# Kernel tuning notes

Hardware: AMD Instinct MI355X
Metric: run time of the kernel (lower is better)

The kernel has to match this reference:

```python
import jax, jax.numpy as jnp
import numpy as np

D_MODEL = 1024
H = 16
D_K = D_MODEL // H
B, S = 4, 2048


def setup_inputs() -> dict:
    key = jax.random.key(0)
    ks = jax.random.split(key, 12)
    s = 1.0 / np.sqrt(D_MODEL)
    inp = {
        "q": jax.random.normal(ks[0], (B, S, D_MODEL), jnp.float32),
        "k": jax.random.normal(ks[1], (B, S, D_MODEL), jnp.float32),
        "v": jax.random.normal(ks[2], (B, S, D_MODEL), jnp.float32),
        "mask": jax.random.randint(ks[3], (1, 1, S, S), 0, 2, jnp.int32),
        # torch nn.Linear convention: weight [out, in], y = x @ W.T + b
        "w_q": jax.random.uniform(ks[4], (D_MODEL, D_MODEL), jnp.float32, -s, s),
        "b_q": jax.random.uniform(ks[5], (D_MODEL,), jnp.float32, -s, s),
        "w_k": jax.random.uniform(ks[6], (D_MODEL, D_MODEL), jnp.float32, -s, s),
        "b_k": jax.random.uniform(ks[7], (D_MODEL,), jnp.float32, -s, s),
        "w_v": jax.random.uniform(ks[8], (D_MODEL, D_MODEL), jnp.float32, -s, s),
        "b_v": jax.random.uniform(ks[9], (D_MODEL,), jnp.float32, -s, s),
        "w_o": jax.random.uniform(ks[10], (D_MODEL, D_MODEL), jnp.float32, -s, s),
        "b_o": jax.random.uniform(ks[11], (D_MODEL,), jnp.float32, -s, s),
    }
    return inp


def _split_heads(x):
    b, s, _ = x.shape
    return x.reshape(b, s, H, D_K).transpose(0, 2, 1, 3)  # [B,H,S,Dk]


def reference(q, k, v, mask, w_q, b_q, w_k, b_k, w_v, b_v, w_o, b_o):
    query = _split_heads(q @ w_q.T + b_q)
    key = _split_heads(k @ w_k.T + b_k)
    value = _split_heads(v @ w_v.T + b_v)
    scores = jnp.einsum("bhqd,bhkd->bhqk", query, key) / jnp.sqrt(
        jnp.asarray(D_K, query.dtype))
    scores = jnp.where(mask == 0, jnp.asarray(-1e9, scores.dtype), scores)
    attn = jax.nn.softmax(scores, axis=-1)  # dropout p=0 (eval) -> identity
    x = jnp.einsum("bhqk,bhkd->bhqd", attn, value)
    x = x.transpose(0, 2, 1, 3).reshape(q.shape[0], -1, H * D_K)
    return x @ w_o.T + b_o
```

## Files before the change

kernel.cpp:

```cpp
#include <hip/hip_runtime.h>

typedef __bf16 bf16_t;
typedef __bf16 bf16x4 __attribute__((ext_vector_type(4)));
typedef __bf16 bf16x8 __attribute__((ext_vector_type(8)));
typedef float f32x4 __attribute__((ext_vector_type(4)));
typedef float f32x16 __attribute__((ext_vector_type(16)));
typedef unsigned int uint;
typedef uint uint4v __attribute__((ext_vector_type(4)));

#define CSCALE 0.18033688011112042f

static __device__ __forceinline__ bf16_t f2bf(float f) {
  unsigned u = __builtin_bit_cast(unsigned, f);
  u = (u + 0x7fff + ((u >> 16) & 1)) >> 16;
  unsigned short h = (unsigned short)u;
  return __builtin_bit_cast(bf16_t, h);
}
static __device__ __forceinline__ uint cvt_pk(float a, float b) {
  uint r;
  asm("v_cvt_pk_bf16_f32 %0, %1, %2" : "=v"(r) : "v"(a), "v"(b));
  return r;
}

#define GLD_LDS(g, l) \
  __builtin_amdgcn_global_load_lds((const __attribute__((address_space(1))) void*)(g), \
                                   (__attribute__((address_space(3))) void*)(l), 16, 0, 0)
#define VMCNT(n) asm volatile("s_waitcnt vmcnt(" #n ")" ::: "memory")
#define RAW_BARRIER() do { __builtin_amdgcn_s_barrier(); __builtin_amdgcn_sched_barrier(0); } while (0)

__global__ void cvt4_f2b(const float* __restrict__ a, const float* __restrict__ b,
                         const float* __restrict__ c, const float* __restrict__ d,
                         bf16_t* __restrict__ oa, bf16_t* __restrict__ ob,
                         bf16_t* __restrict__ oc, bf16_t* __restrict__ od) {
  int i = blockIdx.x * 256 + threadIdx.x;
  const float* src = a;
  bf16_t* dst = oa;
  int w = i >> 18;
  i &= 262143;
  if (w == 1) { src = b; dst = ob; }
  else if (w == 2) { src = c; dst = oc; }
  else if (w == 3) { src = d; dst = od; }
  const float4 f = reinterpret_cast<const float4*>(src)[i];
  bf16x4 o;
  o[0] = f2bf(f.x); o[1] = f2bf(f.y); o[2] = f2bf(f.z); o[3] = f2bf(f.w);
  reinterpret_cast<bf16x4*>(dst)[i] = o;
}

__global__ void mask_bits_k(const int* __restrict__ m, uint* __restrict__ out) {
  int i = blockIdx.x * 256 + threadIdx.x;
  int q = i & 2047, t = i >> 11;
  const int* mrow = m + (size_t)q * 2048 + t * 32;
  uint bits = 0;
#pragma unroll
  for (int j = 0; j < 16; ++j) {
    int r0 = (j & 3) + 8 * (j >> 2);
    bits |= (mrow[r0] ? 1u : 0u) << j;
    bits |= (mrow[r0 + 4] ? 1u : 0u) << (16 + j);
  }
  out[(size_t)t * 2048 + q] = bits;
}

__global__ __launch_bounds__(256, 2) void qkv_gemm(
    const float* __restrict__ qA, const float* __restrict__ kA, const float* __restrict__ vA,
    const bf16_t* __restrict__ wq, const bf16_t* __restrict__ wk, const bf16_t* __restrict__ wv,
    const float* __restrict__ bq, const float* __restrict__ bk, const float* __restrict__ bv,
    bf16_t* __restrict__ Qp, bf16_t* __restrict__ Kp, bf16_t* __restrict__ Vt) {
  constexpr int K = 1024, N = 1024;
  __shared__ __align__(16) float Asf[3][128 * 32];
  __shared__ __align__(16) bf16_t Bs[3][128 * 32];
  const int z = blockIdx.z;
  const float* A = (z == 0) ? qA : (z == 1) ? kA : vA;
  const bf16_t* W = (z == 0) ? wq : (z == 1) ? wk : wv;
  const float* bias = (z == 0) ? bq : (z == 1) ? bk : bv;

  const int tid = threadIdx.x;
  const int lane = tid & 63;
  const int wv_ = tid >> 6;
  const int wm = (wv_ >> 1) * 64, wn = (wv_ & 1) * 64;
  const int l15 = lane & 15, lhi = lane >> 4;
  const int bm = blockIdx.x, bn = blockIdx.y;

  const int rA = tid >> 3;
  const float* gA = A + (size_t)(bm * 128 + rA) * K + ((tid & 7) ^ (rA & 7)) * 4;
  const int rB = tid >> 2;
  const bf16_t* gB = W + (size_t)(bn * 128 + rB) * K + ((tid & 3) ^ (rB & 3)) * 8;

  f32x4 acc[4][4] = {};

  auto STAGE = [&](int t, int buf) {
#pragma unroll
    for (int c2 = 0; c2 < 4; ++c2)
      GLD_LDS(gA + (size_t)c2 * 32 * K + t * 32, (char*)&Asf[buf][0] + c2 * 4096 + wv_ * 1024);
#pragma unroll
    for (int c2 = 0; c2 < 2; ++c2)
      GLD_LDS(gB + (size_t)c2 * 64 * K + t * 32, (char*)&Bs[buf][0] + c2 * 4096 + wv_ * 1024);
  };
  auto COMPUTE = [&](int buf) {
    bf16x8 af[4], bfv[4];
#pragma unroll
    for (int i = 0; i < 4; ++i) {
      int arow = wm + i * 16 + l15;
      f32x4 a0 = *reinterpret_cast<const f32x4*>(
          (const char*)&Asf[buf][0] + arow * 128 + (((2 * lhi) ^ (arow & 7)) * 16));
      f32x4 a1 = *reinterpret_cast<const f32x4*>(
          (const char*)&Asf[buf][0] + arow * 128 + (((2 * lhi + 1) ^ (arow & 7)) * 16));
      uint4v ua;
      ua[0] = cvt_pk(a0[0], a0[1]);
      ua[1] = cvt_pk(a0[2], a0[3]);
      ua[2] = cvt_pk(a1[0], a1[1]);
      ua[3] = cvt_pk(a1[2], a1[3]);
      af[i] = __builtin_bit_cast(bf16x8, ua);
    }
#pragma unroll
    for (int j = 0; j < 4; ++j) {
      int brow = wn + j * 16 + l15;
      bfv[j] = *reinterpret_cast<const bf16x8*>(
          (const char*)&Bs[buf][0] + brow * 64 + ((lhi ^ (brow & 3)) * 16));
    }
#pragma unroll
    for (int i = 0; i < 4; ++i)
#pragma unroll
      for (int j = 0; j < 4; ++j)
        acc[i][j] = __builtin_amdgcn_mfma_f32_16x16x32_bf16(af[i], bfv[j], acc[i][j], 0, 0, 0);
  };

  STAGE(0, 0);
  STAGE(1, 1);
#pragma unroll 1
  for (int tt = 0; tt < 30; tt += 3) {
    VMCNT(6); RAW_BARRIER(); COMPUTE(0); STAGE(tt + 2, 2);
    VMCNT(6); RAW_BARRIER(); COMPUTE(1); STAGE(tt + 3, 0);
    VMCNT(6); RAW_BARRIER(); COMPUTE(2); STAGE(tt + 4, 1);
  }
  VMCNT(6); RAW_BARRIER(); COMPUTE(0);
  VMCNT(0); RAW_BARRIER(); COMPUTE(1);

#pragma unroll
  for (int i = 0; i < 4; ++i) {
#pragma unroll
    for (int j = 0; j < 4; ++j) {
      int n = bn * 128 + wn + j * 16 + l15;
      float bv2 = bias[n];
#pragma unroll
      for (int r = 0; r < 4; ++r) {
        int m = bm * 128 + wm + i * 16 + lhi * 4 + r;
        float val = acc[i][j][r] + bv2;
        if (z == 0) {
          Qp[(size_t)m * N + n] = f2bf(val * CSCALE);
        } else if (z == 1) {
          Kp[(size_t)m * N + n] = f2bf(val);
        } else {
          int b = m >> 11, s = m & 2047;
          Vt[((size_t)b * 1024 + n) * 2048 + s] = f2bf(val);
        }
      }
    }
  }
}

__global__ __launch_bounds__(256, 2) void gemm_o(
    const bf16_t* __restrict__ A, const bf16_t* __restrict__ Bw,
    const float* __restrict__ bias, float* __restrict__ Cout) {
  constexpr int K = 1024, N = 1024;
  __shared__ __align__(16) bf16_t As[3][128 * 32];
  __shared__ __align__(16) bf16_t Bs[3][128 * 32];
  const int tid = threadIdx.x;
  const int lane = tid & 63;
  const int wv_ = tid >> 6;
  const int wm = (wv_ >> 1) * 64, wn = (wv_ & 1) * 64;
  const int l15 = lane & 15, lhi = lane >> 4;
  const int bm = blockIdx.x, bn = blockIdx.y;
  const int rB = tid >> 2;
  const bf16_t* ga = A + (size_t)(bm * 128 + rB) * K + ((tid & 3) ^ (rB & 3)) * 8;
  const bf16_t* gb = Bw + (size_t)(bn * 128 + rB) * K + ((tid & 3) ^ (rB & 3)) * 8;
  f32x4 acc[4][4] = {};

  auto STAGE = [&](int t, int buf) {
#pragma unroll
    for (int c2 = 0; c2 < 2; ++c2) {
      GLD_LDS(ga + (size_t)c2 * 64 * K + t * 32, (char*)&As[buf][0] + c2 * 4096 + wv_ * 1024);
      GLD_LDS(gb + (size_t)c2 * 64 * K + t * 32, (char*)&Bs[buf][0] + c2 * 4096 + wv_ * 1024);
    }
  };
  auto COMPUTE = [&](int buf) {
    bf16x8 af[4], bfv[4];
#pragma unroll
    for (int i = 0; i < 4; ++i) {
      int arow = wm + i * 16 + l15;
      af[i] = *reinterpret_cast<const bf16x8*>(
          (const char*)&As[buf][0] + arow * 64 + ((lhi ^ (arow & 3)) * 16));
    }
#pragma unroll
    for (int j = 0; j < 4; ++j) {
      int brow = wn + j * 16 + l15;
      bfv[j] = *reinterpret_cast<const bf16x8*>(
          (const char*)&Bs[buf][0] + brow * 64 + ((lhi ^ (brow & 3)) * 16));
    }
#pragma unroll
    for (int i = 0; i < 4; ++i)
#pragma unroll
      for (int j = 0; j < 4; ++j)
        acc[i][j] = __builtin_amdgcn_mfma_f32_16x16x32_bf16(af[i], bfv[j], acc[i][j], 0, 0, 0);
  };

  STAGE(0, 0);
  STAGE(1, 1);
#pragma unroll 1
  for (int tt = 0; tt < 30; tt += 3) {
    VMCNT(4); RAW_BARRIER(); COMPUTE(0); STAGE(tt + 2, 2);
    VMCNT(4); RAW_BARRIER(); COMPUTE(1); STAGE(tt + 3, 0);
    VMCNT(4); RAW_BARRIER(); COMPUTE(2); STAGE(tt + 4, 1);
  }
  VMCNT(4); RAW_BARRIER(); COMPUTE(0);
  VMCNT(0); RAW_BARRIER(); COMPUTE(1);

#pragma unroll
  for (int i = 0; i < 4; ++i)
#pragma unroll
    for (int j = 0; j < 4; ++j) {
      int n = bn * 128 + wn + j * 16 + l15;
      float bv2 = bias[n];
#pragma unroll
      for (int r = 0; r < 4; ++r) {
        int m = bm * 128 + wm + i * 16 + lhi * 4 + r;
        Cout[(size_t)m * N + n] = acc[i][j][r] + bv2;
      }
    }
}

static __device__ __forceinline__ f32x16 qk_tile(const bf16_t* Kbuf, const bf16x8 qf[4],
                                                 int l31, int h) {
  f32x16 s = {};
  __builtin_amdgcn_s_setprio(1);
#pragma unroll
  for (int c = 0; c < 4; ++c) {
    bf16x8 kf = *reinterpret_cast<const bf16x8*>(Kbuf + l31 * 64 + ((h + 2 * c) ^ (l31 & 7)) * 8);
    s = __builtin_amdgcn_mfma_f32_32x32x16_bf16(kf, qf[c], s, 0, 0, 0);
  }
  __builtin_amdgcn_s_setprio(0);
  return s;
}

static __device__ __forceinline__ void softmax_tile(
    const f32x16& sv, uint mb, int h, f32x16& o0, f32x16& o1,
    float& mrun, float& lsum, bf16x8& pa0, bf16x8& pa1) {
  const uint mbh = mb >> (h << 4);
  float a0 = fmaxf(fmaxf(sv[0], sv[1]), sv[2]);
  float a1 = fmaxf(fmaxf(sv[3], sv[4]), sv[5]);
  float a2 = fmaxf(fmaxf(sv[6], sv[7]), sv[8]);
  float a3 = fmaxf(fmaxf(sv[9], sv[10]), sv[11]);
  float a4 = fmaxf(fmaxf(sv[12], sv[13]), sv[14]);
  float b0 = fmaxf(fmaxf(a0, a1), a2);
  float mt = fmaxf(fmaxf(b0, fmaxf(a3, a4)), sv[15]);
  if (!__all(mt - mrun <= 8.0f)) {
    float mtf = fmaxf(mt, __shfl_xor(mt, 32));
    float mnew = fmaxf(mrun, mtf);
    float alpha = __builtin_amdgcn_exp2f(mrun - mnew);
    lsum *= alpha;
#pragma unroll
    for (int r = 0; r < 16; ++r) {
      float ar = __shfl(alpha, (r & 3) + 8 * (r >> 2) + 4 * h);
      o0[r] *= ar; o1[r] *= ar;
    }
    mrun = mnew;
  }
  float p[16];
#pragma unroll
  for (int r = 0; r < 16; ++r) {
    float pv = __builtin_amdgcn_exp2f(sv[r] - mrun);
    uint smask = (uint)__builtin_amdgcn_sbfe((int)mbh, r, 1);
    p[r] = __builtin_bit_cast(float, __builtin_bit_cast(uint, pv) & smask);
  }
  float t0 = p[0] + p[1], t1 = p[2] + p[3], t2 = p[4] + p[5], t3 = p[6] + p[7];
  float t4 = p[8] + p[9], t5 = p[10] + p[11], t6 = p[12] + p[13], t7 = p[14] + p[15];
  t0 += t1; t2 += t3; t4 += t5; t6 += t7;
  lsum += (t0 + t2) + (t4 + t6);
  uint dw[8];
#pragma unroll
  for (int i = 0; i < 8; ++i) dw[i] = cvt_pk(p[2 * i], p[2 * i + 1]);
  uint e0 = (uint)__shfl_xor((int)(h ? dw[0] : dw[2]), 32);
  uint e1 = (uint)__shfl_xor((int)(h ? dw[1] : dw[3]), 32);
  uint e2 = (uint)__shfl_xor((int)(h ? dw[4] : dw[6]), 32);
  uint e3 = (uint)__shfl_xor((int)(h ? dw[5] : dw[7]), 32);
  uint4v ua0 = {h ? e0 : dw[0], h ? e1 : dw[1], h ? dw[2] : e0, h ? dw[3] : e1};
  uint4v ua1 = {h ? e2 : dw[4], h ? e3 : dw[5], h ? dw[6] : e2, h ? dw[7] : e3};
  pa0 = __builtin_bit_cast(bf16x8, ua0);
  pa1 = __builtin_bit_cast(bf16x8, ua1);
}

static __device__ __forceinline__ void pv_tile(const bf16_t* Vbuf, bf16x8 pa0, bf16x8 pa1,
                                               int l31, int h, f32x16& o0, f32x16& o1) {
  const int sw = l31 & 3;
  bf16x8 v00 = *reinterpret_cast<const bf16x8*>(Vbuf + l31 * 32 + ((h ^ sw) * 8));
  bf16x8 v01 = *reinterpret_cast<const bf16x8*>(Vbuf + l31 * 32 + (((2 + h) ^ sw) * 8));
  bf16x8 v10 = *reinterpret_cast<const bf16x8*>(Vbuf + (32 + l31) * 32 + ((h ^ sw) * 8));
  bf16x8 v11 = *reinterpret_cast<const bf16x8*>(Vbuf + (32 + l31) * 32 + (((2 + h) ^ sw) * 8));
  __builtin_amdgcn_s_setprio(1);
  o0 = __builtin_amdgcn_mfma_f32_32x32x16_bf16(pa0, v00, o0, 0, 0, 0);
  o0 = __builtin_amdgcn_mfma_f32_32x32x16_bf16(pa1, v01, o0, 0, 0, 0);
  o1 = __builtin_amdgcn_mfma_f32_32x32x16_bf16(pa0, v10, o1, 0, 0, 0);
  o1 = __builtin_amdgcn_mfma_f32_32x32x16_bf16(pa1, v11, o1, 0, 0, 0);
  __builtin_amdgcn_s_setprio(0);
}

__global__ __launch_bounds__(256, 4) void attn_kernel(
    const bf16_t* __restrict__ Qp, const bf16_t* __restrict__ Kp,
    const bf16_t* __restrict__ Vt, const uint* __restrict__ maskbits,
    bf16_t* __restrict__ Xb) {
  constexpr int S = 2048, D = 1024;
  __shared__ __align__(16) bf16_t Ks[2][32][64];
  __shared__ __align__(16) bf16_t Vs[2][64][32];
  const int tid = threadIdx.x;
  const int wv_ = tid >> 6, lane = tid & 63;
  const int l31 = lane & 31, h = lane >> 5;
  const int blk = blockIdx.x;
  const int bh = blk & 63, qt4 = blk >> 6;
  const int b = bh >> 4, hd = bh & 15;
  const int q0 = qt4 * 128 + wv_ * 32;

  const int rK = tid >> 3;
  const bf16_t* gK = Kp + ((size_t)b * S + rK) * D + hd * 64 + ((tid & 7) ^ (rK & 7)) * 8;
  const int rV = tid >> 2;
  const bf16_t* gV = Vt + ((size_t)b * 1024 + hd * 64 + rV) * (size_t)S + ((tid & 3) ^ (rV & 3)) * 8;
  char* ldsK0 = (char*)&Ks[0][0][0] + wv_ * 1024;
  char* ldsK1 = (char*)&Ks[1][0][0] + wv_ * 1024;
  char* ldsV0 = (char*)&Vs[0][0][0] + wv_ * 1024;
  char* ldsV1 = (char*)&Vs[1][0][0] + wv_ * 1024;

  const bf16_t* qbase = Qp + (size_t)(b * S + q0 + l31) * D + hd * 64 + h * 8;
  bf16x8 qf[4];
#pragma unroll
  for (int c = 0; c < 4; ++c)
    qf[c] = *reinterpret_cast<const bf16x8*>(qbase + 16 * c);

  const uint* mbase = maskbits + q0 + l31;

  f32x16 o0 = {}, o1 = {};
  float mrun = 0.f, lsum = 0.f;
  bf16x8 pa0, pa1;

  GLD_LDS(gK, ldsK0);
  GLD_LDS(gK + (size_t)32 * D, ldsK1);
  GLD_LDS(gV, ldsV0);
  uint mb0 = mbase[0];
  __syncthreads();
  {
    f32x16 s = qk_tile(&Ks[0][0][0], qf, l31, h);
    softmax_tile(s, mb0, h, o0, o1, mrun, lsum, pa0, pa1);
  }

  auto body = [&](int j, char* ldsK_st, char* ldsV_st, const bf16_t* Kq,
                  const bf16_t* Vp, bool stageK) {
    if (stageK) GLD_LDS(gK + (size_t)(j + 2) * 32 * D, ldsK_st);
    GLD_LDS(gV + (size_t)(j + 1) * 32, ldsV_st);
    uint mbn = mbase[(size_t)(j + 1) * 2048];
    f32x16 s = qk_tile(Kq, qf, l31, h);
    pv_tile(Vp, pa0, pa1, l31, h, o0, o1);
    softmax_tile(s, mbn, h, o0, o1, mrun, lsum, pa0, pa1);
    __syncthreads();
  };

#pragma unroll 1
  for (int jj = 0; jj < 31; ++jj) {
    const int j = 2 * jj;
    body(j,     ldsK0, ldsV1, &Ks[1][0][0], &Vs[0][0][0], true);
    body(j + 1, ldsK1, ldsV0, &Ks[0][0][0], &Vs[1][0][0], true);
  }
  body(62, ldsK0, ldsV1, &Ks[1][0][0], &Vs[0][0][0], false);
  pv_tile(&Vs[1][0][0], pa0, pa1, l31, h, o0, o1);

  lsum += __shfl_xor(lsum, 32);
  float linv = __builtin_amdgcn_rcpf(lsum);
  bf16_t* xrow = Xb + (size_t)(b * S + q0) * D + hd * 64 + l31;
#pragma unroll
  for (int r = 0; r < 16; ++r) {
    int qrow = (r & 3) + 8 * (r >> 2) + 4 * h;
    float lr = __shfl(linv, qrow);
    xrow[(size_t)qrow * D] = f2bf(o0[r] * lr);
    xrow[(size_t)qrow * D + 32] = f2bf(o1[r] * lr);
  }
}

extern "C" void kernel_launch(void* const* d_in, const int* in_sizes, int n_in,
                              void* d_out, int out_size, void* d_ws, size_t ws_size,
                              hipStream_t stream) {
  const float* q = (const float*)d_in[0];
  const float* k = (const float*)d_in[1];
  const float* v = (const float*)d_in[2];
  const int* mask = (const int*)d_in[3];
  const float* w_q = (const float*)d_in[4];
  const float* b_q = (const float*)d_in[5];
  const float* w_k = (const float*)d_in[6];
  const float* b_k = (const float*)d_in[7];
  const float* w_v = (const float*)d_in[8];
  const float* b_v = (const float*)d_in[9];
  const float* w_o = (const float*)d_in[10];
  const float* b_o = (const float*)d_in[11];

  char* ws = (char*)d_ws;
  const size_t SZ = (size_t)8192 * 1024 * 2;
  bf16_t* Qp = (bf16_t*)(ws + 0 * SZ);
  bf16_t* Kp = (bf16_t*)(ws + 1 * SZ);
  bf16_t* Vt = (bf16_t*)(ws + 2 * SZ);
  bf16_t* Xb = (bf16_t*)(ws + 3 * SZ);
  uint* maskB = (uint*)(ws + 4 * SZ);
  bf16_t* wqb = (bf16_t*)(ws + 4 * SZ + 8388608);
  bf16_t* wkb = wqb + 1048576;
  bf16_t* wvb = wkb + 1048576;
  bf16_t* wob = wvb + 1048576;

  cvt4_f2b<<<4096, 256, 0, stream>>>(w_q, w_k, w_v, w_o, wqb, wkb, wvb, wob);
  mask_bits_k<<<512, 256, 0, stream>>>(mask, maskB);

  dim3 g3(64, 8, 3);
  qkv_gemm<<<g3, 256, 0, stream>>>(q, k, v, wqb, wkb, wvb, b_q, b_k, b_v, Qp, Kp, Vt);
  attn_kernel<<<1024, 256, 0, stream>>>(Qp, Kp, Vt, maskB, Xb);
  gemm_o<<<dim3(64, 8), 256, 0, stream>>>(Xb, wob, b_o, (float*)d_out);
}
```

Measured before the change: 251.7 us.

## Widen GEMM tiles to 128x256 and convert A to bf16 before LDS

Both projection GEMMs move from 128x128 to 128x256 block tiles, with each wave computing 64x128, so every staged A element feeds twice as many MFMAs and grid sizes halve. In the QKV GEMM the fp32 activations are loaded into registers, converted to bf16 once and written to LDS. This replaces staging fp32 through LDS and converting on every fragment read, which halves A's LDS footprint and cuts repeated conversions. The V-transpose epilogue now writes packed 4-element bf16 vectors. The costs are twice the accumulator registers, a register-staged A path that can expose global latency, and fewer blocks available to fill the GPU.

```diff
diff --git a/kernel.cpp b/kernel.cpp
--- a/kernel.cpp
+++ b/kernel.cpp
@@ -6,6 +6,7 @@
 typedef float f32x4 __attribute__((ext_vector_type(4)));
 typedef float f32x16 __attribute__((ext_vector_type(16)));
 typedef unsigned int uint;
+typedef uint uint2v __attribute__((ext_vector_type(2)));
 typedef uint uint4v __attribute__((ext_vector_type(4)));
 
 #define CSCALE 0.18033688011112042f
@@ -26,7 +27,8 @@
   __builtin_amdgcn_global_load_lds((const __attribute__((address_space(1))) void*)(g), \
                                    (__attribute__((address_space(3))) void*)(l), 16, 0, 0)
 #define VMCNT(n) asm volatile("s_waitcnt vmcnt(" #n ")" ::: "memory")
-#define RAW_BARRIER() do { __builtin_amdgcn_s_barrier(); __builtin_amdgcn_sched_barrier(0); } while (0)
+#define LGKM0() asm volatile("s_waitcnt lgkmcnt(0)" ::: "memory")
+#define BARRIER() do { __builtin_amdgcn_s_barrier(); __builtin_amdgcn_sched_barrier(0); } while (0)
 
 __global__ void cvt4_f2b(const float* __restrict__ a, const float* __restrict__ b,
                          const float* __restrict__ c, const float* __restrict__ d,
@@ -65,9 +67,9 @@
     const bf16_t* __restrict__ wq, const bf16_t* __restrict__ wk, const bf16_t* __restrict__ wv,
     const float* __restrict__ bq, const float* __restrict__ bk, const float* __restrict__ bv,
     bf16_t* __restrict__ Qp, bf16_t* __restrict__ Kp, bf16_t* __restrict__ Vt) {
-  constexpr int K = 1024, N = 1024;
-  __shared__ __align__(16) float Asf[3][128 * 32];
-  __shared__ __align__(16) bf16_t Bs[3][128 * 32];
+  constexpr int K = 1024;
+  __shared__ __align__(16) bf16_t AsB[2][128 * 32];
+  __shared__ __align__(16) bf16_t BsB[3][256 * 32];
   const int z = blockIdx.z;
   const float* A = (z == 0) ? qA : (z == 1) ? kA : vA;
   const bf16_t* W = (z == 0) ? wq : (z == 1) ? wk : wv;
@@ -76,51 +78,168 @@
   const int tid = threadIdx.x;
   const int lane = tid & 63;
   const int wv_ = tid >> 6;
-  const int wm = (wv_ >> 1) * 64, wn = (wv_ & 1) * 64;
+  const int wm = (wv_ & 1) * 64, wn = (wv_ >> 1) * 128;
   const int l15 = lane & 15, lhi = lane >> 4;
   const int bm = blockIdx.x, bn = blockIdx.y;
 
-  const int rA = tid >> 3;
-  const float* gA = A + (size_t)(bm * 128 + rA) * K + ((tid & 7) ^ (rA & 7)) * 4;
-  const int rB = tid >> 2;
-  const bf16_t* gB = W + (size_t)(bn * 128 + rB) * K + ((tid & 3) ^ (rB & 3)) * 8;
-
-  f32x4 acc[4][4] = {};
-
-  auto STAGE = [&](int t, int buf) {
+  const int arow0 = tid >> 3;
+  const int acol = tid & 7;
+  const float* gA = A + (size_t)(bm * 128 + arow0) * K + acol * 4;
+  const int brows = tid >> 2;
+  const bf16_t* gB = W + (size_t)(bn * 256 + brows) * K + ((tid & 3) ^ (brows & 3)) * 8;
+
+  f32x4 acc[4][8] = {};
+  f32x4 rA0[4], rA1[4];
+
+  auto A_LOAD = [&](int t, f32x4* R) {
+#pragma unroll
+    for (int L = 0; L < 4; ++L)
+      R[L] = *reinterpret_cast<const f32x4*>(gA + (size_t)L * 32 * K + t * 32);
+  };
+  auto A_WRITE = [&](const f32x4* R, int buf) {
+#pragma unroll
+    for (int L = 0; L < 4; ++L) {
+      int row = arow0 + L * 32;
+      uint2v u;
+      u[0] = cvt_pk(R[L][0], R[L][1]);
+      u[1] = cvt_pk(R[L][2], R[L][3]);
+      char* p = (char*)&AsB[buf][0] + row * 64 + (((acol >> 1) ^ (row & 3)) * 16) + (acol & 1) * 8;
+      *reinterpret_cast<uint2v*>(p) = u;
+    }
+  };
+  auto B_STAGE = [&](int t, int buf) {
 #pragma unroll
     for (int c2 = 0; c2 < 4; ++c2)
-      GLD_LDS(gA + (size_t)c2 * 32 * K + t * 32, (char*)&Asf[buf][0] + c2 * 4096 + wv_ * 1024);
-#pragma unroll
-    for (int c2 = 0; c2 < 2; ++c2)
-      GLD_LDS(gB + (size_t)c2 * 64 * K + t * 32, (char*)&Bs[buf][0] + c2 * 4096 + wv_ * 1024);
-  };
-  auto COMPUTE = [&](int buf) {
-    bf16x8 af[4], bfv[4];
+      GLD_LDS(gB + (size_t)c2 * 64 * K + t * 32, (char*)&BsB[buf][0] + c2 * 4096 + wv_ * 1024);
+  };
+  auto COMPUTE = [&](int ba, int bb) {
+    bf16x8 af[4], bfv[8];
 #pragma unroll
     for (int i = 0; i < 4; ++i) {
       int arow = wm + i * 16 + l15;
-      f32x4 a0 = *reinterpret_cast<const f32x4*>(
-          (const char*)&Asf[buf][0] + arow * 128 + (((2 * lhi) ^ (arow & 7)) * 16));
-      f32x4 a1 = *reinterpret_cast<const f32x4*>(
-          (const char*)&Asf[buf][0] + arow * 128 + (((2 * lhi + 1) ^ (arow & 7)) * 16));
-      uint4v ua;
-      ua[0] = cvt_pk(a0[0], a0[1]);
-      ua[1] = cvt_pk(a0[2], a0[3]);
-      ua[2] = cvt_pk(a1[0], a1[1]);
-      ua[3] = cvt_pk(a1[2], a1[3]);
-      af[i] = __builtin_bit_cast(bf16x8, ua);
-    }
-#pragma unroll
-    for (int j = 0; j < 4; ++j) {
-      int brow = wn + j * 16 + l15;
+      af[i] = *reinterpret_cast<const bf16x8*>(
+          (const char*)&AsB[ba][0] + arow * 64 + ((lhi ^ (arow & 3)) * 16));
+    }
+#pragma unroll
+    for (int j = 0; j < 8; ++j) {
+      int br = wn + j * 16 + l15;
       bfv[j] = *reinterpret_cast<const bf16x8*>(
-          (const char*)&Bs[buf][0] + brow * 64 + ((lhi ^ (brow & 3)) * 16));
+          (const char*)&BsB[bb][0] + br * 64 + ((lhi ^ (br & 3)) * 16));
     }
 #pragma unroll
     for (int i = 0; i < 4; ++i)
 #pragma unroll
-      for (int j = 0; j < 4; ++j)
+      for (int j = 0; j < 8; ++j)
+        acc[i][j] = __builtin_amdgcn_mfma_f32_16x16x32_bf16(af[i], bfv[j], acc[i][j], 0, 0, 0);
+  };
+
+#define QSTEP(T, RL, RW, BAW, BAC, BBC, BBS) \
+  A_LOAD((T) + 2, RL); B_STAGE((T) + 2, BBS); \
+  COMPUTE(BAC, BBC); \
+  VMCNT(8); \
+  A_WRITE(RW, BAW); \
+  LGKM0(); BARRIER();
+
+  A_LOAD(0, rA0); B_STAGE(0, 0);
+  A_LOAD(1, rA1); B_STAGE(1, 1);
+  VMCNT(8);
+  A_WRITE(rA0, 0);
+  LGKM0(); BARRIER();
+
+#pragma unroll 1
+  for (int t6 = 0; t6 < 30; t6 += 6) {
+    QSTEP(t6 + 0, rA0, rA1, 1, 0, 0, 2)
+    QSTEP(t6 + 1, rA1, rA0, 0, 1, 1, 0)
+    QSTEP(t6 + 2, rA0, rA1, 1, 0, 2, 1)
+    QSTEP(t6 + 3, rA1, rA0, 0, 1, 0, 2)
+    QSTEP(t6 + 4, rA0, rA1, 1, 0, 1, 0)
+    QSTEP(t6 + 5, rA1, rA0, 0, 1, 2, 1)
+  }
+  COMPUTE(0, 0);
+  VMCNT(4);
+  A_WRITE(rA1, 1);
+  VMCNT(0);
+  LGKM0(); BARRIER();
+  COMPUTE(1, 1);
+
+  if (z == 2) {
+    const int b = (bm * 128) >> 11;
+    const int s0 = (bm * 128) & 2047;
+    bf16_t* vb = Vt + ((size_t)b * 1024 + bn * 256 + wn + l15) * 2048 + s0 + wm + lhi * 4;
+#pragma unroll
+    for (int j = 0; j < 8; ++j) {
+      float bv2 = bias[bn * 256 + wn + j * 16 + l15];
+#pragma unroll
+      for (int i = 0; i < 4; ++i) {
+        bf16x4 pk;
+#pragma unroll
+        for (int r = 0; r < 4; ++r) pk[r] = f2bf(acc[i][j][r] + bv2);
+        *reinterpret_cast<bf16x4*>(vb + (size_t)(j * 16) * 2048 + i * 16) = pk;
+      }
+    }
+  } else {
+    bf16_t* O = (z == 0) ? Qp : Kp;
+    const float scale = (z == 0) ? CSCALE : 1.0f;
+#pragma unroll
+    for (int i = 0; i < 4; ++i) {
+#pragma unroll
+      for (int j = 0; j < 8; ++j) {
+        int n = bn * 256 + wn + j * 16 + l15;
+        float bv2 = bias[n];
+#pragma unroll
+        for (int r = 0; r < 4; ++r) {
+          int m = bm * 128 + wm + i * 16 + lhi * 4 + r;
+          O[(size_t)m * 1024 + n] = f2bf((acc[i][j][r] + bv2) * scale);
+        }
+      }
+    }
+  }
+#undef QSTEP
+}
+
+__global__ __launch_bounds__(256, 2) void gemm_o(
+    const bf16_t* __restrict__ A, const bf16_t* __restrict__ Bw,
+    const float* __restrict__ bias, float* __restrict__ Cout) {
+  constexpr int K = 1024;
+  __shared__ __align__(16) bf16_t As[3][128 * 32];
+  __shared__ __align__(16) bf16_t Bs[3][256 * 32];
+  const int tid = threadIdx.x;
+  const int lane = tid & 63;
+  const int wv_ = tid >> 6;
+  const int wm = (wv_ & 1) * 64, wn = (wv_ >> 1) * 128;
+  const int l15 = lane & 15, lhi = lane >> 4;
+  const int bm = blockIdx.x, bn = blockIdx.y;
+  const int rws = tid >> 2;
+  const bf16_t* ga = A + (size_t)(bm * 128 + rws) * K + ((tid & 3) ^ (rws & 3)) * 8;
+  const bf16_t* gb = Bw + (size_t)(bn * 256 + rws) * K + ((tid & 3) ^ (rws & 3)) * 8;
+  f32x4 acc[4][8] = {};
+
+  auto STAGE = [&](int t, int buf) {
+#pragma unroll
+    for (int c2 = 0; c2 < 2; ++c2)
+      GLD_LDS(ga + (size_t)c2 * 64 * K + t * 32, (char*)&As[buf][0] + c2 * 4096 + wv_ * 1024);
+#pragma unroll
+    for (int c2 = 0; c2 < 4; ++c2)
+      GLD_LDS(gb + (size_t)c2 * 64 * K + t * 32, (char*)&Bs[buf][0] + c2 * 4096 + wv_ * 1024);
+  };
+  auto COMPUTE = [&](int buf) {
+    bf16x8 af[4], bfv[8];
+#pragma unroll
+    for (int i = 0; i < 4; ++i) {
+      int arow = wm + i * 16 + l15;
+      af[i] = *reinterpret_cast<const bf16x8*>(
+          (const char*)&As[buf][0] + arow * 64 + ((lhi ^ (arow & 3)) * 16));
+    }
+#pragma unroll
+    for (int j = 0; j < 8; ++j) {
+      int br = wn + j * 16 + l15;
+      bfv[j] = *reinterpret_cast<const bf16x8*>(
+          (const char*)&Bs[buf][0] + br * 64 + ((lhi ^ (br & 3)) * 16));
+    }
+#pragma unroll
+    for (int i = 0; i < 4; ++i)
+#pragma unroll
+      for (int j = 0; j < 8; ++j)
         acc[i][j] = __builtin_amdgcn_mfma_f32_16x16x32_bf16(af[i], bfv[j], acc[i][j], 0, 0, 0);
   };
 
@@ -128,102 +247,23 @@
   STAGE(1, 1);
 #pragma unroll 1
   for (int tt = 0; tt < 30; tt += 3) {
-    VMCNT(6); RAW_BARRIER(); COMPUTE(0); STAGE(tt + 2, 2);
-    VMCNT(6); RAW_BARRIER(); COMPUTE(1); STAGE(tt + 3, 0);
-    VMCNT(6); RAW_BARRIER(); COMPUTE(2); STAGE(tt + 4, 1);
-  }
-  VMCNT(6); RAW_BARRIER(); COMPUTE(0);
-  VMCNT(0); RAW_BARRIER(); COMPUTE(1);
-
-#pragma unroll
-  for (int i = 0; i < 4; ++i) {
-#pragma unroll
-    for (int j = 0; j < 4; ++j) {
-      int n = bn * 128 + wn + j * 16 + l15;
+    VMCNT(6); BARRIER(); COMPUTE(0); STAGE(tt + 2, 2);
+    VMCNT(6); BARRIER(); COMPUTE(1); STAGE(tt + 3, 0);
+    VMCNT(6); BARRIER(); COMPUTE(2); STAGE(tt + 4, 1);
+  }
+  VMCNT(6); BARRIER(); COMPUTE(0);
+  VMCNT(0); BARRIER(); COMPUTE(1);
+
+#pragma unroll
+  for (int i = 0; i < 4; ++i)
+#pragma unroll
+    for (int j = 0; j < 8; ++j) {
+      int n = bn * 256 + wn + j * 16 + l15;
       float bv2 = bias[n];
 #pragma unroll
       for (int r = 0; r < 4; ++r) {
         int m = bm * 128 + wm + i * 16 + lhi * 4 + r;
-        float val = acc[i][j][r] + bv2;
-        if (z == 0) {
-          Qp[(size_t)m * N + n] = f2bf(val * CSCALE);
-        } else if (z == 1) {
-          Kp[(size_t)m * N + n] = f2bf(val);
-        } else {
-          int b = m >> 11, s = m & 2047;
-          Vt[((size_t)b * 1024 + n) * 2048 + s] = f2bf(val);
-        }
-      }
-    }
-  }
-}
-
-__global__ __launch_bounds__(256, 2) void gemm_o(
-    const bf16_t* __restrict__ A, const bf16_t* __restrict__ Bw,
-    const float* __restrict__ bias, float* __restrict__ Cout) {
-  constexpr int K = 1024, N = 1024;
-  __shared__ __align__(16) bf16_t As[3][128 * 32];
-  __shared__ __align__(16) bf16_t Bs[3][128 * 32];
-  const int tid = threadIdx.x;
-  const int lane = tid & 63;
-  const int wv_ = tid >> 6;
-  const int wm = (wv_ >> 1) * 64, wn = (wv_ & 1) * 64;
-  const int l15 = lane & 15, lhi = lane >> 4;
-  const int bm = blockIdx.x, bn = blockIdx.y;
-  const int rB = tid >> 2;
-  const bf16_t* ga = A + (size_t)(bm * 128 + rB) * K + ((tid & 3) ^ (rB & 3)) * 8;
-  const bf16_t* gb = Bw + (size_t)(bn * 128 + rB) * K + ((tid & 3) ^ (rB & 3)) * 8;
-  f32x4 acc[4][4] = {};
-
-  auto STAGE = [&](int t, int buf) {
-#pragma unroll
-    for (int c2 = 0; c2 < 2; ++c2) {
-      GLD_LDS(ga + (size_t)c2 * 64 * K + t * 32, (char*)&As[buf][0] + c2 * 4096 + wv_ * 1024);
-      GLD_LDS(gb + (size_t)c2 * 64 * K + t * 32, (char*)&Bs[buf][0] + c2 * 4096 + wv_ * 1024);
-    }
-  };
-  auto COMPUTE = [&](int buf) {
-    bf16x8 af[4], bfv[4];
-#pragma unroll
-    for (int i = 0; i < 4; ++i) {
-      int arow = wm + i * 16 + l15;
-      af[i] = *reinterpret_cast<const bf16x8*>(
-          (const char*)&As[buf][0] + arow * 64 + ((lhi ^ (arow & 3)) * 16));
-    }
-#pragma unroll
-    for (int j = 0; j < 4; ++j) {
-      int brow = wn + j * 16 + l15;
-      bfv[j] = *reinterpret_cast<const bf16x8*>(
-          (const char*)&Bs[buf][0] + brow * 64 + ((lhi ^ (brow & 3)) * 16));
-    }
-#pragma unroll
-    for (int i = 0; i < 4; ++i)
-#pragma unroll
-      for (int j = 0; j < 4; ++j)
-        acc[i][j] = __builtin_amdgcn_mfma_f32_16x16x32_bf16(af[i], bfv[j], acc[i][j], 0, 0, 0);
-  };
-
-  STAGE(0, 0);
-  STAGE(1, 1);
-#pragma unroll 1
-  for (int tt = 0; tt < 30; tt += 3) {
-    VMCNT(4); RAW_BARRIER(); COMPUTE(0); STAGE(tt + 2, 2);
-    VMCNT(4); RAW_BARRIER(); COMPUTE(1); STAGE(tt + 3, 0);
-    VMCNT(4); RAW_BARRIER(); COMPUTE(2); STAGE(tt + 4, 1);
-  }
-  VMCNT(4); RAW_BARRIER(); COMPUTE(0);
-  VMCNT(0); RAW_BARRIER(); COMPUTE(1);
-
-#pragma unroll
-  for (int i = 0; i < 4; ++i)
-#pragma unroll
-    for (int j = 0; j < 4; ++j) {
-      int n = bn * 128 + wn + j * 16 + l15;
-      float bv2 = bias[n];
-#pragma unroll
-      for (int r = 0; r < 4; ++r) {
-        int m = bm * 128 + wm + i * 16 + lhi * 4 + r;
-        Cout[(size_t)m * N + n] = acc[i][j][r] + bv2;
+        Cout[(size_t)m * 1024 + n] = acc[i][j][r] + bv2;
       }
     }
 }
@@ -412,8 +452,8 @@
   cvt4_f2b<<<4096, 256, 0, stream>>>(w_q, w_k, w_v, w_o, wqb, wkb, wvb, wob);
   mask_bits_k<<<512, 256, 0, stream>>>(mask, maskB);
 
-  dim3 g3(64, 8, 3);
+  dim3 g3(64, 4, 3);
   qkv_gemm<<<g3, 256, 0, stream>>>(q, k, v, wqb, wkb, wvb, b_q, b_k, b_v, Qp, Kp, Vt);
   attn_kernel<<<1024, 256, 0, stream>>>(Qp, Kp, Vt, maskB, Xb);
-  gemm_o<<<dim3(64, 8), 256, 0, stream>>>(Xb, wob, b_o, (float*)d_out);
-}
+  gemm_o<<<dim3(64, 4), 256, 0, stream>>>(Xb, wob, b_o, (float*)d_out);
+}
```

New measurement: 237.1 us. -5.8%, faster.
